# Optimization experiments

Measured on AMD Instinct MI355X. Metric: run time of the kernel, lower is better.

Reference implementation:

```python
import jax, jax.numpy as jnp
jax.config.update("jax_enable_x64", True)
import numpy as np

HASH_PRIMES = [2654435761, 2246822519, 3266489917, 2028178513, 1220703125, 1610612741, 805306457, 402653189, 3674653429, 2860486313, 1073676287, 2971215073, 1500450271, 3267000013, 2654435789, 4049292737, 2246822531, 3266489927, 2028178519, 1220703133, 1610612743, 805306459, 402653191, 3674653433, 2654435771, 2246822527, 3266489933, 2028178529, 1220703137, 1610612747, 805306463, 402653197, 3674653441, 2860486319, 1073676293, 2971215077, 1500450281, 3267000017, 2654435801, 4049292743, 2246822537, 3266489939, 2028178531, 1220703143, 1610612753, 805306467, 402653201, 3674653447]

VOCAB = 1024
BYTE_DIM = 128
NUM_TABLES = 32
BUCKETS = 131072
EMBED = 32
HIDDEN = 512
NUM_LAYERS = 2
HASH_SEED = 0
BATCH, SEQ = 8, 4096


def _generate_patterns(num_tables, max_offset):
    # 'default' branch of the original _generate_patterns
    patterns = [(o,) for o in range(1, min(num_tables // 4 + 1, 9))]
    pairs = [(1, 2), (2, 3), (3, 4), (1, 3), (2, 4), (1, 4), (1, 5), (2, 5), (3, 5), (1, 6), (2, 6), (1, 7)]
    for p in pairs:
        if len(patterns) >= num_tables:
            break
        patterns.append(p)
    trigrams = [(1, 2, 3), (1, 2, 4), (1, 3, 5), (2, 3, 4)]
    for t in trigrams:
        if len(patterns) >= num_tables:
            break
        patterns.append(t)
    off = 8
    while len(patterns) < num_tables:
        patterns.append((1, off))
        off += 1
    return patterns[:num_tables]

PATTERNS = _generate_patterns(NUM_TABLES, 8)


def _hash_indices(tokens):
    """tokens: [B,S] int64 -> [T,B,S] int64 bucket indices (polynomial XOR hash)."""
    B, S = tokens.shape
    idx = []
    for t, pattern in enumerate(PATTERNS):
        h = jnp.zeros((B, S), dtype=jnp.int64)
        for k, off in enumerate(pattern):
            prime = jnp.int64(HASH_PRIMES[(t * 3 + k + HASH_SEED) % len(HASH_PRIMES)])
            # shift right by `off` along seq, zero-fill front (off >= 1 always)
            shifted = jnp.pad(tokens[:, : S - off], ((0, 0), (off, 0)))
            h = h ^ (shifted * prime)
        idx.append(h % BUCKETS)
    return jnp.stack(idx, axis=0)  # [T,B,S]


def _layer_norm(x, w, b, eps=1e-5):
    mu = jnp.mean(x, axis=-1, keepdims=True)
    var = jnp.var(x, axis=-1, keepdims=True)
    return (x - mu) * jax.lax.rsqrt(var + eps) * w + b


def setup_inputs() -> dict:
    key = jax.random.key(0)
    ks = jax.random.split(key, 12)
    tokens = jax.random.randint(ks[0], (BATCH, SEQ), 0, VOCAB, dtype=jnp.int64)
    feat_dim = BYTE_DIM + NUM_TABLES * EMBED
    return {
        "tokens": tokens,
        "byte_embed": jax.random.normal(ks[1], (VOCAB, BYTE_DIM), jnp.float32),
        "hash_tables": 0.02 * jax.random.normal(ks[2], (NUM_TABLES, BUCKETS, EMBED), jnp.float32),
        "in_w": jax.random.normal(ks[3], (feat_dim, HIDDEN), jnp.float32) / np.sqrt(feat_dim),
        "in_b": jnp.zeros((HIDDEN,), jnp.float32),
        "res_w": jax.random.normal(ks[4], (NUM_LAYERS, HIDDEN, HIDDEN), jnp.float32) / np.sqrt(HIDDEN),
        "res_b": jnp.zeros((NUM_LAYERS, HIDDEN), jnp.float32),
        "ln_w": jnp.ones((NUM_LAYERS, HIDDEN), jnp.float32),
        "ln_b": jnp.zeros((NUM_LAYERS, HIDDEN), jnp.float32),
        "out_w": jax.random.normal(ks[5], (HIDDEN, VOCAB), jnp.float32) / np.sqrt(HIDDEN),
        "out_b": jnp.zeros((VOCAB,), jnp.float32),
    }


def reference(tokens, byte_embed, hash_tables, in_w, in_b, res_w, res_b, ln_w, ln_b, out_w, out_b):
    B, S = tokens.shape
    T = hash_tables.shape[0]
    idx = _hash_indices(tokens)  # [T,B,S]
    # one fused gather over all tables: [T,B,S,E]
    hashed = hash_tables[jnp.arange(T)[:, None, None], idx]
    hash_feats = jnp.transpose(hashed, (1, 2, 0, 3)).reshape(B, S, T * EMBED)
    byte_feats = byte_embed[tokens]  # [B,S,BYTE_DIM]
    feats = jnp.concatenate([byte_feats, hash_feats], axis=-1)
    h = feats @ in_w + in_b  # input_proj -> [B,S,HIDDEN]
    for l in range(NUM_LAYERS):  # ResBlock: relu(Wx+b) + x, then LayerNorm
        hh = jax.nn.relu(h @ res_w[l] + res_b[l]) + h
        h = _layer_norm(hh, ln_w[l], ln_b[l])
    return h @ out_w + out_b  # logits [B,S,VOCAB]
```

## Files before the change

kernel.cpp:

```cpp
#include <hip/hip_runtime.h>

typedef unsigned short u16;
typedef unsigned int   u32;
typedef __bf16  bf16x8  __attribute__((ext_vector_type(8)));
typedef float   floatx4 __attribute__((ext_vector_type(4)));

#define BATCH 8
#define SEQ 4096
#define NTOK (BATCH*SEQ)
#define BYTE_DIM 128
#define NUM_TABLES 32
#define BUCKETS 131072
#define EMBED 32
#define FEAT 1152
#define HIDDEN 512
#define VOCAB 1024

__constant__ u32 PRIMES[48] = {
  2654435761u, 2246822519u, 3266489917u, 2028178513u, 1220703125u, 1610612741u,
  805306457u, 402653189u, 3674653429u, 2860486313u, 1073676287u, 2971215073u,
  1500450271u, 3267000013u, 2654435789u, 4049292737u, 2246822531u, 3266489927u,
  2028178519u, 1220703133u, 1610612743u, 805306459u, 402653191u, 3674653433u,
  2654435771u, 2246822527u, 3266489933u, 2028178529u, 1220703137u, 1610612747u,
  805306463u, 402653197u, 3674653441u, 2860486319u, 1073676293u, 2971215077u,
  1500450281u, 3267000017u, 2654435801u, 4049292743u, 2246822537u, 3266489939u,
  2028178531u, 1220703143u, 1610612753u, 805306467u, 402653201u, 3674653447u };

__constant__ int PAT_LEN[32] = {1,1,1,1,1,1,1,1,
                                2,2,2,2,2,2,2,2,2,2,2,2,
                                3,3,3,3,
                                2,2,2,2,2,2,2,2};
__constant__ int PAT_OFF[32][3] = {
  {1,0,0},{2,0,0},{3,0,0},{4,0,0},{5,0,0},{6,0,0},{7,0,0},{8,0,0},
  {1,2,0},{2,3,0},{3,4,0},{1,3,0},{2,4,0},{1,4,0},{1,5,0},{2,5,0},
  {3,5,0},{1,6,0},{2,6,0},{1,7,0},
  {1,2,3},{1,2,4},{1,3,5},{2,3,4},
  {1,8,0},{1,9,0},{1,10,0},{1,11,0},{1,12,0},{1,13,0},{1,14,0},{1,15,0}};

__device__ __forceinline__ u16 f2bf(float f) {
  u32 u = __builtin_bit_cast(u32, f);
  u = u + 0x7FFFu + ((u >> 16) & 1u);
  return (u16)(u >> 16);
}
__device__ __forceinline__ float bf2f(u16 h) {
  return __builtin_bit_cast(float, (u32)h << 16);
}

__device__ __forceinline__ void gld16(const void* g, void* l) {
  __builtin_amdgcn_global_load_lds(
      (const __attribute__((address_space(1))) void*)g,
      (__attribute__((address_space(3))) void*)l, 16, 0, 0);
}

__global__ __launch_bounds__(256) void transpose_bf16(
    const float* __restrict__ src, u16* __restrict__ dst, int K, int N) {
  __shared__ float tile[32][33];
  int bx = blockIdx.x;
  int by = blockIdx.y;
  int tx = threadIdx.x & 31, ty = threadIdx.x >> 5;
  #pragma unroll
  for (int i = 0; i < 32; i += 8)
    tile[ty + i][tx] = src[(size_t)(by*32 + ty + i) * N + bx*32 + tx];
  __syncthreads();
  #pragma unroll
  for (int i = 0; i < 32; i += 8)
    dst[(size_t)(bx*32 + ty + i) * K + by*32 + tx] = f2bf(tile[tx][ty + i]);
}

__global__ __launch_bounds__(256) void feats_kernel(
    const int* __restrict__ tokens, const float* __restrict__ byte_embed,
    const float* __restrict__ hash_tables, u16* __restrict__ feats) {
  int gid = blockIdx.x * 256 + threadIdx.x;
  int g = gid / 144;
  int c = gid - g * 144;
  int b = g >> 12, s = g & 4095;
  const float* src;
  int col;
  if (c < 16) {
    int tok = tokens[g];
    col = c * 8;
    src = byte_embed + (size_t)tok * BYTE_DIM + col;
  } else {
    int hc = c - 16;
    int tt = hc >> 2;
    int e0 = (hc & 3) * 8;
    unsigned h = 0;
    int len = PAT_LEN[tt];
    #pragma unroll
    for (int k = 0; k < 3; ++k) {
      if (k < len) {
        int off = PAT_OFF[tt][k];
        int sp = s - off;
        unsigned tok = (sp >= 0) ? (unsigned)tokens[(b << 12) + sp] : 0u;
        unsigned prime = PRIMES[(tt * 3 + k) % 48] & 0x1FFFFu;
        h ^= (tok * prime) & 0x1FFFFu;
      }
    }
    src = hash_tables + ((size_t)tt * BUCKETS + (h & 0x1FFFFu)) * EMBED + e0;
    col = BYTE_DIM + tt * EMBED + e0;
  }
  float4 v0 = *(const float4*)src;
  float4 v1 = *(const float4*)(src + 4);
  union { u16 s[8]; uint4 v; } p;
  p.s[0]=f2bf(v0.x); p.s[1]=f2bf(v0.y); p.s[2]=f2bf(v0.z); p.s[3]=f2bf(v0.w);
  p.s[4]=f2bf(v1.x); p.s[5]=f2bf(v1.y); p.s[6]=f2bf(v1.z); p.s[7]=f2bf(v1.w);
  *(uint4*)&feats[(size_t)g * FEAT + col] = p.v;
}

template <int EPI>
__global__ __launch_bounds__(256) void gemm_bf16(
    const u16* __restrict__ A, const u16* __restrict__ BT,
    const float* __restrict__ bias, const u16* __restrict__ RES,
    void* __restrict__ Cout, int M, int N, int K) {
  __shared__ __align__(16) u16 As[128 * 32];
  __shared__ __align__(16) u16 Bs[128 * 32];
  const int t = threadIdx.x;
  const int w = t >> 6, l = t & 63;
  const int m0 = blockIdx.y * 128;
  const int n0 = blockIdx.x * 128;
  const int wm = (w >> 1) * 64, wn = (w & 1) * 64;
  const int r16 = l & 15, hk = (l >> 4) * 8;

  floatx4 acc[4][4];
  #pragma unroll
  for (int mi = 0; mi < 4; ++mi)
    #pragma unroll
    for (int ni = 0; ni < 4; ++ni)
      acc[mi][ni] = (floatx4){0.f, 0.f, 0.f, 0.f};

  for (int k0 = 0; k0 < K; k0 += 32) {
    #pragma unroll
    for (int j = 0; j < 2; ++j) {
      int c = j * 256 + t;
      int row = c >> 2, q = c & 3;
      gld16(A  + (size_t)(m0 + row) * K + k0 + q * 8, &As[c * 8]);
      gld16(BT + (size_t)(n0 + row) * K + k0 + q * 8, &Bs[c * 8]);
    }
    __syncthreads();
    bf16x8 af[4], bfr[4];
    #pragma unroll
    for (int mi = 0; mi < 4; ++mi)
      af[mi] = *(const bf16x8*)&As[(wm + mi * 16 + r16) * 32 + hk];
    #pragma unroll
    for (int ni = 0; ni < 4; ++ni)
      bfr[ni] = *(const bf16x8*)&Bs[(wn + ni * 16 + r16) * 32 + hk];
    #pragma unroll
    for (int mi = 0; mi < 4; ++mi)
      #pragma unroll
      for (int ni = 0; ni < 4; ++ni)
        acc[mi][ni] = __builtin_amdgcn_mfma_f32_16x16x32_bf16(
            af[mi], bfr[ni], acc[mi][ni], 0, 0, 0);
    __syncthreads();
  }

  const int q4 = (l >> 4) * 4;
  #pragma unroll
  for (int mi = 0; mi < 4; ++mi) {
    #pragma unroll
    for (int ni = 0; ni < 4; ++ni) {
      int col = n0 + wn + ni * 16 + r16;
      float bn = bias[col];
      int rowb = m0 + wm + mi * 16 + q4;
      #pragma unroll
      for (int r = 0; r < 4; ++r) {
        float v = acc[mi][ni][r] + bn;
        size_t off = (size_t)(rowb + r) * N + col;
        if (EPI == 0) {
          ((u16*)Cout)[off] = f2bf(v);
        } else if (EPI == 1) {
          v = fmaxf(v, 0.f) + bf2f(RES[off]);
          ((float*)Cout)[off] = v;
        } else {
          ((float*)Cout)[off] = v;
        }
      }
    }
  }
}

__global__ __launch_bounds__(256) void ln_kernel(
    const float* __restrict__ X, const float* __restrict__ lw,
    const float* __restrict__ lb, u16* __restrict__ Y) {
  int t = threadIdx.x;
  int wv = t >> 6, l = t & 63;
  int row = blockIdx.x * 4 + wv;
  const float* x = X + (size_t)row * HIDDEN + l * 8;
  float4 v0 = *(const float4*)x;
  float4 v1 = *(const float4*)(x + 4);
  float xs[8] = {v0.x, v0.y, v0.z, v0.w, v1.x, v1.y, v1.z, v1.w};
  float s1 = 0.f, s2 = 0.f;
  #pragma unroll
  for (int i = 0; i < 8; ++i) { s1 += xs[i]; s2 += xs[i] * xs[i]; }
  #pragma unroll
  for (int d = 1; d < 64; d <<= 1) {
    s1 += __shfl_xor(s1, d);
    s2 += __shfl_xor(s2, d);
  }
  float mu = s1 * (1.f / HIDDEN);
  float var = s2 * (1.f / HIDDEN) - mu * mu;
  float inv = rsqrtf(fmaxf(var, 0.f) + 1e-5f);
  int c = l * 8;
  union { u16 s[8]; uint4 v; } p;
  #pragma unroll
  for (int i = 0; i < 8; ++i)
    p.s[i] = f2bf((xs[i] - mu) * inv * lw[c + i] + lb[c + i]);
  *(uint4*)&Y[(size_t)row * HIDDEN + c] = p.v;
}

extern "C" void kernel_launch(void* const* d_in, const int* in_sizes, int n_in,
                              void* d_out, int out_size, void* d_ws, size_t ws_size,
                              hipStream_t stream) {
  const int*   tokens      = (const int*)  d_in[0];
  const float* byte_embed  = (const float*)d_in[1];
  const float* hash_tables = (const float*)d_in[2];
  const float* in_w        = (const float*)d_in[3];
  const float* in_b        = (const float*)d_in[4];
  const float* res_w       = (const float*)d_in[5];
  const float* res_b       = (const float*)d_in[6];
  const float* ln_w        = (const float*)d_in[7];
  const float* ln_b        = (const float*)d_in[8];
  const float* out_w       = (const float*)d_in[9];
  const float* out_b       = (const float*)d_in[10];
  float* out = (float*)d_out;

  char* ws = (char*)d_ws;
  u16* wT_in  = (u16*)ws; ws += (size_t)HIDDEN * FEAT * 2;
  u16* wT_r0  = (u16*)ws; ws += (size_t)HIDDEN * HIDDEN * 2;
  u16* wT_r1  = (u16*)ws; ws += (size_t)HIDDEN * HIDDEN * 2;
  u16* wT_out = (u16*)ws; ws += (size_t)VOCAB * HIDDEN * 2;
  u16* feats  = (u16*)ws; ws += (size_t)NTOK * FEAT * 2;
  u16* hA     = (u16*)ws; ws += (size_t)NTOK * HIDDEN * 2;
  u16* hB     = (u16*)ws; ws += (size_t)NTOK * HIDDEN * 2;
  float* gg   = (float*)ws;

  transpose_bf16<<<dim3(HIDDEN/32, FEAT/32),  256, 0, stream>>>(in_w,  wT_in,  FEAT,   HIDDEN);
  transpose_bf16<<<dim3(HIDDEN/32, HIDDEN/32),256, 0, stream>>>(res_w, wT_r0, HIDDEN, HIDDEN);
  transpose_bf16<<<dim3(HIDDEN/32, HIDDEN/32),256, 0, stream>>>(res_w + (size_t)HIDDEN*HIDDEN, wT_r1, HIDDEN, HIDDEN);
  transpose_bf16<<<dim3(VOCAB/32,  HIDDEN/32),256, 0, stream>>>(out_w, wT_out, HIDDEN, VOCAB);

  feats_kernel<<<(NTOK * 144) / 256, 256, 0, stream>>>(tokens, byte_embed, hash_tables, feats);

  gemm_bf16<0><<<dim3(HIDDEN/128, NTOK/128), 256, 0, stream>>>(
      feats, wT_in, in_b, nullptr, hA, NTOK, HIDDEN, FEAT);

  gemm_bf16<1><<<dim3(HIDDEN/128, NTOK/128), 256, 0, stream>>>(
      hA, wT_r0, res_b, hA, gg, NTOK, HIDDEN, HIDDEN);
  ln_kernel<<<NTOK/4, 256, 0, stream>>>(gg, ln_w, ln_b, hB);

  gemm_bf16<1><<<dim3(HIDDEN/128, NTOK/128), 256, 0, stream>>>(
      hB, wT_r1, res_b + HIDDEN, hB, gg, NTOK, HIDDEN, HIDDEN);
  ln_kernel<<<NTOK/4, 256, 0, stream>>>(gg, ln_w + HIDDEN, ln_b + HIDDEN, hA);

  gemm_bf16<2><<<dim3(VOCAB/128, NTOK/128), 256, 0, stream>>>(
      hA, wT_out, out_b, nullptr, out, NTOK, VOCAB, HIDDEN);
}
```

Measured before the change: 911.3 us.

## Fuse residual GEMM with LayerNorm, double-buffer GEMM LDS, merge transposes

Replaces each residual-block GEMM plus separate LayerNorm with a single kernel where a 512-thread block computes full 128x512 output rows, applies bias, ReLU and the residual, then reduces row statistics through shared memory and writes the normalized bf16 output. This removes the fp32 intermediate round trip and two launches per layer. The generic GEMM gains LDS double buffering so the next tile's loads can overlap compute, and the four weight-transpose launches become one. The fused kernel holds many accumulator registers per thread with only 256 blocks, which risks low occupancy.

```diff
diff --git a/kernel.cpp b/kernel.cpp
--- a/kernel.cpp
+++ b/kernel.cpp
@@ -52,11 +52,30 @@
       (__attribute__((address_space(3))) void*)l, 16, 0, 0);
 }
 
-__global__ __launch_bounds__(256) void transpose_bf16(
-    const float* __restrict__ src, u16* __restrict__ dst, int K, int N) {
+__global__ __launch_bounds__(256) void transpose_all(
+    const float* __restrict__ in_w, const float* __restrict__ res_w,
+    const float* __restrict__ out_w,
+    u16* __restrict__ wT_in, u16* __restrict__ wT_r0,
+    u16* __restrict__ wT_r1, u16* __restrict__ wT_out) {
   __shared__ float tile[32][33];
-  int bx = blockIdx.x;
-  int by = blockIdx.y;
+  int tid = blockIdx.x;
+  const float* src; u16* dst; int K, N, bx, by;
+  if (tid < 576) {
+    src = in_w;  dst = wT_in;  K = FEAT;   N = HIDDEN;
+    bx = tid & 15; by = tid >> 4;
+  } else if (tid < 832) {
+    int id = tid - 576;
+    src = res_w; dst = wT_r0;  K = HIDDEN; N = HIDDEN;
+    bx = id & 15; by = id >> 4;
+  } else if (tid < 1088) {
+    int id = tid - 832;
+    src = res_w + (size_t)HIDDEN * HIDDEN; dst = wT_r1; K = HIDDEN; N = HIDDEN;
+    bx = id & 15; by = id >> 4;
+  } else {
+    int id = tid - 1088;
+    src = out_w; dst = wT_out; K = HIDDEN; N = VOCAB;
+    bx = id & 31; by = id >> 5;
+  }
   int tx = threadIdx.x & 31, ty = threadIdx.x >> 5;
   #pragma unroll
   for (int i = 0; i < 32; i += 8)
@@ -110,10 +129,10 @@
 template <int EPI>
 __global__ __launch_bounds__(256) void gemm_bf16(
     const u16* __restrict__ A, const u16* __restrict__ BT,
-    const float* __restrict__ bias, const u16* __restrict__ RES,
+    const float* __restrict__ bias,
     void* __restrict__ Cout, int M, int N, int K) {
-  __shared__ __align__(16) u16 As[128 * 32];
-  __shared__ __align__(16) u16 Bs[128 * 32];
+  __shared__ __align__(16) u16 As[2][128 * 32];
+  __shared__ __align__(16) u16 Bs[2][128 * 32];
   const int t = threadIdx.x;
   const int w = t >> 6, l = t & 63;
   const int m0 = blockIdx.y * 128;
@@ -128,22 +147,29 @@
     for (int ni = 0; ni < 4; ++ni)
       acc[mi][ni] = (floatx4){0.f, 0.f, 0.f, 0.f};
 
-  for (int k0 = 0; k0 < K; k0 += 32) {
+  auto stage = [&](int b, int k0) {
     #pragma unroll
     for (int j = 0; j < 2; ++j) {
       int c = j * 256 + t;
       int row = c >> 2, q = c & 3;
-      gld16(A  + (size_t)(m0 + row) * K + k0 + q * 8, &As[c * 8]);
-      gld16(BT + (size_t)(n0 + row) * K + k0 + q * 8, &Bs[c * 8]);
-    }
-    __syncthreads();
+      gld16(A  + (size_t)(m0 + row) * K + k0 + q * 8, &As[b][c * 8]);
+      gld16(BT + (size_t)(n0 + row) * K + k0 + q * 8, &Bs[b][c * 8]);
+    }
+  };
+
+  stage(0, 0);
+  __syncthreads();
+  int cur = 0;
+  const int nk = K >> 5;
+  for (int kt = 0; kt < nk; ++kt) {
+    if (kt + 1 < nk) stage(cur ^ 1, (kt + 1) * 32);
     bf16x8 af[4], bfr[4];
     #pragma unroll
     for (int mi = 0; mi < 4; ++mi)
-      af[mi] = *(const bf16x8*)&As[(wm + mi * 16 + r16) * 32 + hk];
+      af[mi] = *(const bf16x8*)&As[cur][(wm + mi * 16 + r16) * 32 + hk];
     #pragma unroll
     for (int ni = 0; ni < 4; ++ni)
-      bfr[ni] = *(const bf16x8*)&Bs[(wn + ni * 16 + r16) * 32 + hk];
+      bfr[ni] = *(const bf16x8*)&Bs[cur][(wn + ni * 16 + r16) * 32 + hk];
     #pragma unroll
     for (int mi = 0; mi < 4; ++mi)
       #pragma unroll
@@ -151,6 +177,7 @@
         acc[mi][ni] = __builtin_amdgcn_mfma_f32_16x16x32_bf16(
             af[mi], bfr[ni], acc[mi][ni], 0, 0, 0);
     __syncthreads();
+    cur ^= 1;
   }
 
   const int q4 = (l >> 4) * 4;
@@ -167,9 +194,6 @@
         size_t off = (size_t)(rowb + r) * N + col;
         if (EPI == 0) {
           ((u16*)Cout)[off] = f2bf(v);
-        } else if (EPI == 1) {
-          v = fmaxf(v, 0.f) + bf2f(RES[off]);
-          ((float*)Cout)[off] = v;
         } else {
           ((float*)Cout)[off] = v;
         }
@@ -178,33 +202,118 @@
   }
 }
 
-__global__ __launch_bounds__(256) void ln_kernel(
-    const float* __restrict__ X, const float* __restrict__ lw,
-    const float* __restrict__ lb, u16* __restrict__ Y) {
-  int t = threadIdx.x;
-  int wv = t >> 6, l = t & 63;
-  int row = blockIdx.x * 4 + wv;
-  const float* x = X + (size_t)row * HIDDEN + l * 8;
-  float4 v0 = *(const float4*)x;
-  float4 v1 = *(const float4*)(x + 4);
-  float xs[8] = {v0.x, v0.y, v0.z, v0.w, v1.x, v1.y, v1.z, v1.w};
-  float s1 = 0.f, s2 = 0.f;
-  #pragma unroll
-  for (int i = 0; i < 8; ++i) { s1 += xs[i]; s2 += xs[i] * xs[i]; }
-  #pragma unroll
-  for (int d = 1; d < 64; d <<= 1) {
-    s1 += __shfl_xor(s1, d);
-    s2 += __shfl_xor(s2, d);
-  }
-  float mu = s1 * (1.f / HIDDEN);
-  float var = s2 * (1.f / HIDDEN) - mu * mu;
-  float inv = rsqrtf(fmaxf(var, 0.f) + 1e-5f);
-  int c = l * 8;
-  union { u16 s[8]; uint4 v; } p;
-  #pragma unroll
-  for (int i = 0; i < 8; ++i)
-    p.s[i] = f2bf((xs[i] - mu) * inv * lw[c + i] + lb[c + i]);
-  *(uint4*)&Y[(size_t)row * HIDDEN + c] = p.v;
+__global__ __launch_bounds__(512) void fused_layer(
+    const u16* __restrict__ A, const u16* __restrict__ WT,
+    const float* __restrict__ bias,
+    const float* __restrict__ lw, const float* __restrict__ lb,
+    u16* __restrict__ Y) {
+  __shared__ __align__(16) u16 As[2][128 * 32];
+  __shared__ __align__(16) u16 Bs[2][512 * 32];
+  __shared__ float red1[128][4];
+  __shared__ float red2[128][4];
+  __shared__ float2 muinv[128];
+
+  const int t = threadIdx.x;
+  const int w = t >> 6, l = t & 63;
+  const int m0 = blockIdx.x * 128;
+  const int wm = (w >> 2) * 64;
+  const int wn = (w & 3) * 128;
+  const int r16 = l & 15, hk = (l >> 4) * 8, q4 = (l >> 4) * 4;
+
+  floatx4 acc[4][8];
+  #pragma unroll
+  for (int mi = 0; mi < 4; ++mi)
+    #pragma unroll
+    for (int ni = 0; ni < 8; ++ni)
+      acc[mi][ni] = (floatx4){0.f, 0.f, 0.f, 0.f};
+
+  auto stage = [&](int b, int k0) {
+    {
+      int row = t >> 2, q = t & 3;
+      gld16(A + (size_t)(m0 + row) * HIDDEN + k0 + q * 8, &As[b][t * 8]);
+    }
+    #pragma unroll
+    for (int j = 0; j < 4; ++j) {
+      int c = j * 512 + t;
+      int row = c >> 2, q = c & 3;
+      gld16(WT + (size_t)row * HIDDEN + k0 + q * 8, &Bs[b][c * 8]);
+    }
+  };
+
+  stage(0, 0);
+  __syncthreads();
+  int cur = 0;
+  #pragma unroll 1
+  for (int kt = 0; kt < 16; ++kt) {
+    if (kt < 15) stage(cur ^ 1, (kt + 1) * 32);
+    bf16x8 af[4], bfr[8];
+    #pragma unroll
+    for (int mi = 0; mi < 4; ++mi)
+      af[mi] = *(const bf16x8*)&As[cur][(wm + mi * 16 + r16) * 32 + hk];
+    #pragma unroll
+    for (int ni = 0; ni < 8; ++ni)
+      bfr[ni] = *(const bf16x8*)&Bs[cur][(wn + ni * 16 + r16) * 32 + hk];
+    #pragma unroll
+    for (int mi = 0; mi < 4; ++mi)
+      #pragma unroll
+      for (int ni = 0; ni < 8; ++ni)
+        acc[mi][ni] = __builtin_amdgcn_mfma_f32_16x16x32_bf16(
+            af[mi], bfr[ni], acc[mi][ni], 0, 0, 0);
+    __syncthreads();
+    cur ^= 1;
+  }
+
+  float bn[8], lwv[8], lbv[8];
+  #pragma unroll
+  for (int ni = 0; ni < 8; ++ni) {
+    int col = wn + ni * 16 + r16;
+    bn[ni] = bias[col]; lwv[ni] = lw[col]; lbv[ni] = lb[col];
+  }
+  #pragma unroll
+  for (int mi = 0; mi < 4; ++mi) {
+    #pragma unroll
+    for (int r = 0; r < 4; ++r) {
+      int rl = wm + mi * 16 + q4 + r;
+      size_t gbase = (size_t)(m0 + rl) * HIDDEN;
+      float s1 = 0.f, s2 = 0.f;
+      #pragma unroll
+      for (int ni = 0; ni < 8; ++ni) {
+        float rv = bf2f(A[gbase + wn + ni * 16 + r16]);
+        float x = fmaxf(acc[mi][ni][r] + bn[ni], 0.f) + rv;
+        acc[mi][ni][r] = x;
+        s1 += x; s2 += x * x;
+      }
+      #pragma unroll
+      for (int d = 1; d < 16; d <<= 1) {
+        s1 += __shfl_xor(s1, d);
+        s2 += __shfl_xor(s2, d);
+      }
+      if (r16 == 0) { red1[rl][w & 3] = s1; red2[rl][w & 3] = s2; }
+    }
+  }
+  __syncthreads();
+  if (t < 128) {
+    float s1 = red1[t][0] + red1[t][1] + red1[t][2] + red1[t][3];
+    float s2 = red2[t][0] + red2[t][1] + red2[t][2] + red2[t][3];
+    float mu = s1 * (1.f / HIDDEN);
+    float var = s2 * (1.f / HIDDEN) - mu * mu;
+    muinv[t] = make_float2(mu, rsqrtf(fmaxf(var, 0.f) + 1e-5f));
+  }
+  __syncthreads();
+  #pragma unroll
+  for (int mi = 0; mi < 4; ++mi) {
+    #pragma unroll
+    for (int r = 0; r < 4; ++r) {
+      int rl = wm + mi * 16 + q4 + r;
+      float2 mv = muinv[rl];
+      size_t gbase = (size_t)(m0 + rl) * HIDDEN;
+      #pragma unroll
+      for (int ni = 0; ni < 8; ++ni) {
+        float y = (acc[mi][ni][r] - mv.x) * mv.y * lwv[ni] + lbv[ni];
+        Y[gbase + wn + ni * 16 + r16] = f2bf(y);
+      }
+    }
+  }
 }
 
 extern "C" void kernel_launch(void* const* d_in, const int* in_sizes, int n_in,
@@ -230,27 +339,21 @@
   u16* wT_out = (u16*)ws; ws += (size_t)VOCAB * HIDDEN * 2;
   u16* feats  = (u16*)ws; ws += (size_t)NTOK * FEAT * 2;
   u16* hA     = (u16*)ws; ws += (size_t)NTOK * HIDDEN * 2;
-  u16* hB     = (u16*)ws; ws += (size_t)NTOK * HIDDEN * 2;
-  float* gg   = (float*)ws;
-
-  transpose_bf16<<<dim3(HIDDEN/32, FEAT/32),  256, 0, stream>>>(in_w,  wT_in,  FEAT,   HIDDEN);
-  transpose_bf16<<<dim3(HIDDEN/32, HIDDEN/32),256, 0, stream>>>(res_w, wT_r0, HIDDEN, HIDDEN);
-  transpose_bf16<<<dim3(HIDDEN/32, HIDDEN/32),256, 0, stream>>>(res_w + (size_t)HIDDEN*HIDDEN, wT_r1, HIDDEN, HIDDEN);
-  transpose_bf16<<<dim3(VOCAB/32,  HIDDEN/32),256, 0, stream>>>(out_w, wT_out, HIDDEN, VOCAB);
+  u16* hB     = (u16*)ws;
+
+  transpose_all<<<1600, 256, 0, stream>>>(in_w, res_w, out_w,
+                                          wT_in, wT_r0, wT_r1, wT_out);
 
   feats_kernel<<<(NTOK * 144) / 256, 256, 0, stream>>>(tokens, byte_embed, hash_tables, feats);
 
   gemm_bf16<0><<<dim3(HIDDEN/128, NTOK/128), 256, 0, stream>>>(
-      feats, wT_in, in_b, nullptr, hA, NTOK, HIDDEN, FEAT);
-
-  gemm_bf16<1><<<dim3(HIDDEN/128, NTOK/128), 256, 0, stream>>>(
-      hA, wT_r0, res_b, hA, gg, NTOK, HIDDEN, HIDDEN);
-  ln_kernel<<<NTOK/4, 256, 0, stream>>>(gg, ln_w, ln_b, hB);
-
-  gemm_bf16<1><<<dim3(HIDDEN/128, NTOK/128), 256, 0, stream>>>(
-      hB, wT_r1, res_b + HIDDEN, hB, gg, NTOK, HIDDEN, HIDDEN);
-  ln_kernel<<<NTOK/4, 256, 0, stream>>>(gg, ln_w + HIDDEN, ln_b + HIDDEN, hA);
+      feats, wT_in, in_b, hA, NTOK, HIDDEN, FEAT);
+
+  fused_layer<<<NTOK/128, 512, 0, stream>>>(hA, wT_r0, res_b, ln_w, ln_b, hB);
+
+  fused_layer<<<NTOK/128, 512, 0, stream>>>(hB, wT_r1, res_b + HIDDEN,
+                                            ln_w + HIDDEN, ln_b + HIDDEN, hA);
 
   gemm_bf16<2><<<dim3(VOCAB/128, NTOK/128), 256, 0, stream>>>(
-      hA, wT_out, out_b, nullptr, out, NTOK, VOCAB, HIDDEN);
-}
+      hA, wT_out, out_b, out, NTOK, VOCAB, HIDDEN);
+}
```

Result: faster. 870.5 us (-4.5%).
